# Kernel tuning notes

Hardware: AMD Instinct MI355X
Metric: run time of the kernel (lower is better)

## Reference

```python
import jax, jax.numpy as jnp
import numpy as np

T, H, E, K, I = 512, 2048, 16, 4, 1408
NS = 2
IS = I * NS  # shared-expert intermediate
SCALE = 1.0  # routed_scaling_factor


def setup_inputs() -> dict:
    key = jax.random.key(0)
    ks = jax.random.split(key, 6)
    init = lambda k, shape, fan: (jax.random.normal(k, shape, jnp.float32) * (fan ** -0.5))
    return {
        "hidden_states": jax.random.normal(ks[0], (T, H), jnp.float32),
        "gate_w": init(ks[1], (E, H), H),            # router weight
        "w_gate_up": init(ks[2], (E, 2 * I, H), H),  # merged gate_up per expert
        "w_down": init(ks[3], (E, H, I), I),         # down proj per expert
        "shared_gate_up": init(ks[4], (2 * IS, H), H),
        "shared_down": init(ks[5], (H, IS), IS),
    }


def reference(hidden_states, gate_w, w_gate_up, w_down, shared_gate_up, shared_down):
    x = hidden_states  # [T, H]
    # ---- shared experts (BailingMoEMLP: SiluAndMul) ----
    gu = x @ shared_gate_up.T                      # [T, 2*IS]
    g, u = jnp.split(gu, 2, axis=-1)
    shared = (jax.nn.silu(g) * u) @ shared_down.T  # [T, H]
    # ---- router: softmax scores, top-k, renormalize (norm_topk_prob=True) ----
    logits = x @ gate_w.T                          # [T, E]
    probs = jax.nn.softmax(logits, axis=-1)
    topk_w, topk_idx = jax.lax.top_k(probs, K)     # [T, K]
    topk_w = topk_w / jnp.sum(topk_w, axis=-1, keepdims=True)
    # dense combine weights [T, E] (scatter of top-k weights)
    t_idx = jnp.arange(x.shape[0])[:, None]
    cw = jnp.zeros((x.shape[0], E), x.dtype).at[t_idx, topk_idx].set(topk_w)
    # ---- experts: dense batched GEMM over all experts, weighted combine ----
    gu_e = jnp.einsum('th,eih->tei', x, w_gate_up)   # [T, E, 2I]
    g_e, u_e = jnp.split(gu_e, 2, axis=-1)
    h_e = jax.nn.silu(g_e) * u_e                     # [T, E, I]
    routed = jnp.einsum('tei,ehi,te->th', h_e, w_down, cw) * SCALE
    return routed + shared
```

## Files before the change

### kernel.cpp

```cpp
#include <hip/hip_runtime.h>
#include <hip/hip_bf16.h>
#include <math.h>

#define T_TOK 512
#define H_DIM 2048
#define E_NUM 16
#define K_TOP 4
#define I_DIM 1408
#define IS_DIM 2816

typedef __bf16 bf16;
typedef __attribute__((ext_vector_type(8))) __bf16 bf16x8;
typedef __attribute__((ext_vector_type(4))) float f32x4;

#define BM 64
#define BN 64
#define BK 64

__device__ inline bf16x8 cvt8(const float* __restrict__ p) {
    const f32x4 a = *(const f32x4*)(p);
    const f32x4 b = *(const f32x4*)(p + 4);
    bf16x8 r;
    r[0] = (bf16)a[0]; r[1] = (bf16)a[1]; r[2] = (bf16)a[2]; r[3] = (bf16)a[3];
    r[4] = (bf16)b[0]; r[5] = (bf16)b[1]; r[6] = (bf16)b[2]; r[7] = (bf16)b[3];
    return r;
}

__global__ __launch_bounds__(64) void router_kernel(
    const float* __restrict__ x, const float* __restrict__ gw,
    int* __restrict__ counts, int* __restrict__ tok_id, float* __restrict__ tok_w)
{
    int t = blockIdx.x;
    int lane = threadIdx.x;
    float acc[E_NUM];
#pragma unroll
    for (int e = 0; e < E_NUM; e++) acc[e] = 0.f;
    for (int h = lane; h < H_DIM; h += 64) {
        float xv = x[t * H_DIM + h];
#pragma unroll
        for (int e = 0; e < E_NUM; e++) acc[e] += xv * gw[e * H_DIM + h];
    }
#pragma unroll
    for (int e = 0; e < E_NUM; e++) {
#pragma unroll
        for (int off = 32; off; off >>= 1) acc[e] += __shfl_xor(acc[e], off);
    }
    if (lane == 0) {
        float m = acc[0];
#pragma unroll
        for (int e = 1; e < E_NUM; e++) m = fmaxf(m, acc[e]);
        float p[E_NUM];
#pragma unroll
        for (int e = 0; e < E_NUM; e++) p[e] = __expf(acc[e] - m);
        int sel[K_TOP];
        float pw[K_TOP];
        float wsum = 0.f;
        bool used[E_NUM];
#pragma unroll
        for (int e = 0; e < E_NUM; e++) used[e] = false;
        for (int k = 0; k < K_TOP; k++) {
            int best = 0;
            float bv = -1.f;
            for (int e = 0; e < E_NUM; e++) {
                if (!used[e] && p[e] > bv) { bv = p[e]; best = e; }
            }
            used[best] = true;
            sel[k] = best;
            pw[k] = bv;
            wsum += bv;
        }
        float inv = 1.f / wsum;
        for (int k = 0; k < K_TOP; k++) {
            int e = sel[k];
            int pos = atomicAdd(&counts[e], 1);
            tok_id[e * T_TOK + pos] = t;
            tok_w[e * T_TOK + pos] = pw[k] * inv;
        }
    }
}

template <bool GATHER>
__global__ __launch_bounds__(256) void gateup_kernel(
    const float* __restrict__ X,
    const float* __restrict__ W,
    long w_expert_stride,
    int pair_off_rows,
    bf16* __restrict__ Hout,
    long h_expert_stride,
    int ldh,
    const int* __restrict__ counts,
    const int* __restrict__ tok_id,
    const float* __restrict__ tok_w)
{
    int e = blockIdx.z;
    int n0 = blockIdx.x * BN;
    int m0 = blockIdx.y * BM;
    int count;
    if constexpr (GATHER) count = counts[e]; else count = T_TOK;
    if (m0 >= count) return;

    const float* Wg = W + (long)e * w_expert_stride;
    const float* Wu = Wg + (long)pair_off_rows * H_DIM;
    bf16* Ho = Hout + (long)e * h_expert_stride;
    const int* tid_p = nullptr;
    const float* tw_p = nullptr;
    if constexpr (GATHER) {
        tid_p = tok_id + e * T_TOK;
        tw_p = tok_w + e * T_TOK;
    }

    __shared__ bf16 sA[BM * BK];
    __shared__ bf16 sG[BN * BK];
    __shared__ bf16 sU[BN * BK];

    int tidx = threadIdx.x;
    int lane = tidx & 63;
    int wv = tidx >> 6;
    int wm = wv >> 1, wn = wv & 1;

    f32x4 accG[2][2], accU[2][2];
#pragma unroll
    for (int i = 0; i < 2; i++)
#pragma unroll
        for (int j = 0; j < 2; j++) {
            accG[i][j] = (f32x4){0.f, 0.f, 0.f, 0.f};
            accU[i][j] = (f32x4){0.f, 0.f, 0.f, 0.f};
        }

    long arow_off[2], wrow_off[2];
    int lds_off[2];
#pragma unroll
    for (int c2 = 0; c2 < 2; c2++) {
        int c = tidx + c2 * 256;
        int row = c >> 3, col8 = c & 7;
        int tok;
        if constexpr (GATHER) {
            int idx = m0 + row;
            tok = (idx < count) ? tid_p[idx] : tid_p[0];
        } else {
            tok = m0 + row;
        }
        arow_off[c2] = (long)tok * H_DIM + col8 * 8;
        wrow_off[c2] = (long)(n0 + row) * H_DIM + col8 * 8;
        lds_off[c2] = row * BK + ((col8 ^ (row & 7)) << 3);
    }

    const int ktiles = H_DIM / BK;
    for (int kt = 0; kt < ktiles; kt++) {
        int k0 = kt * BK;
#pragma unroll
        for (int c2 = 0; c2 < 2; c2++) {
            *(bf16x8*)&sA[lds_off[c2]] = cvt8(&X[arow_off[c2] + k0]);
            *(bf16x8*)&sG[lds_off[c2]] = cvt8(&Wg[wrow_off[c2] + k0]);
            *(bf16x8*)&sU[lds_off[c2]] = cvt8(&Wu[wrow_off[c2] + k0]);
        }
        __syncthreads();
        int quad = lane >> 4, l16 = lane & 15;
        bf16x8 aF[2][2], gF[2][2], uF[2][2];
#pragma unroll
        for (int mt = 0; mt < 2; mt++) {
            int r = wm * 32 + mt * 16 + l16;
            int rb = r * BK, rx = r & 7;
#pragma unroll
            for (int ks = 0; ks < 2; ks++)
                aF[mt][ks] = *(const bf16x8*)&sA[rb + (((ks * 4 + quad) ^ rx) << 3)];
        }
#pragma unroll
        for (int nt = 0; nt < 2; nt++) {
            int r = wn * 32 + nt * 16 + l16;
            int rb = r * BK, rx = r & 7;
#pragma unroll
            for (int ks = 0; ks < 2; ks++) {
                gF[nt][ks] = *(const bf16x8*)&sG[rb + (((ks * 4 + quad) ^ rx) << 3)];
                uF[nt][ks] = *(const bf16x8*)&sU[rb + (((ks * 4 + quad) ^ rx) << 3)];
            }
        }
#pragma unroll
        for (int ks = 0; ks < 2; ks++)
#pragma unroll
            for (int mt = 0; mt < 2; mt++)
#pragma unroll
                for (int nt = 0; nt < 2; nt++) {
                    accG[mt][nt] = __builtin_amdgcn_mfma_f32_16x16x32_bf16(aF[mt][ks], gF[nt][ks], accG[mt][nt], 0, 0, 0);
                    accU[mt][nt] = __builtin_amdgcn_mfma_f32_16x16x32_bf16(aF[mt][ks], uF[nt][ks], accU[mt][nt], 0, 0, 0);
                }
        __syncthreads();
    }

    int quad = lane >> 4, l16 = lane & 15;
#pragma unroll
    for (int mt = 0; mt < 2; mt++) {
#pragma unroll
        for (int r = 0; r < 4; r++) {
            int row = m0 + wm * 32 + mt * 16 + quad * 4 + r;
            if (row < count) {
                float wgt = 1.f;
                if constexpr (GATHER) wgt = tw_p[row];
#pragma unroll
                for (int nt = 0; nt < 2; nt++) {
                    int col = n0 + wn * 32 + nt * 16 + l16;
                    float g = accG[mt][nt][r];
                    float u = accU[mt][nt][r];
                    float sig = 1.f / (1.f + __expf(-g));
                    float h = g * sig * u * wgt;
                    Ho[(long)row * ldh + col] = (bf16)h;
                }
            }
        }
    }
}

template <bool GATHER>
__global__ __launch_bounds__(256) void down_kernel(
    const bf16* __restrict__ Hin,
    long h_expert_stride, int ldh, int Kdim,
    const float* __restrict__ W,
    long w_expert_stride,
    float* __restrict__ out,
    const int* __restrict__ counts,
    const int* __restrict__ tok_id)
{
    int e = blockIdx.z;
    int n0 = blockIdx.x * BN;
    int m0 = blockIdx.y * BM;
    int count;
    if constexpr (GATHER) count = counts[e]; else count = T_TOK;
    if (m0 >= count) return;

    const bf16* A = Hin + (long)e * h_expert_stride;
    const float* B = W + (long)e * w_expert_stride;
    const int* tid_p = nullptr;
    if constexpr (GATHER) tid_p = tok_id + e * T_TOK;

    __shared__ bf16 sA[BM * BK];
    __shared__ bf16 sB[BN * BK];

    int tidx = threadIdx.x;
    int lane = tidx & 63;
    int wv = tidx >> 6;
    int wm = wv >> 1, wn = wv & 1;

    f32x4 acc[2][2];
#pragma unroll
    for (int i = 0; i < 2; i++)
#pragma unroll
        for (int j = 0; j < 2; j++) acc[i][j] = (f32x4){0.f, 0.f, 0.f, 0.f};

    long arow_off[2], brow_off[2];
    int lds_off[2];
#pragma unroll
    for (int c2 = 0; c2 < 2; c2++) {
        int c = tidx + c2 * 256;
        int row = c >> 3, col8 = c & 7;
        arow_off[c2] = (long)(m0 + row) * ldh + col8 * 8;
        brow_off[c2] = (long)(n0 + row) * Kdim + col8 * 8;
        lds_off[c2] = row * BK + ((col8 ^ (row & 7)) << 3);
    }

    const int ktiles = Kdim / BK;
    for (int kt = 0; kt < ktiles; kt++) {
        int k0 = kt * BK;
#pragma unroll
        for (int c2 = 0; c2 < 2; c2++) {
            *(bf16x8*)&sA[lds_off[c2]] = *(const bf16x8*)&A[arow_off[c2] + k0];
            *(bf16x8*)&sB[lds_off[c2]] = cvt8(&B[brow_off[c2] + k0]);
        }
        __syncthreads();
        int quad = lane >> 4, l16 = lane & 15;
        bf16x8 aF[2][2], bF[2][2];
#pragma unroll
        for (int mt = 0; mt < 2; mt++) {
            int r = wm * 32 + mt * 16 + l16;
            int rb = r * BK, rx = r & 7;
#pragma unroll
            for (int ks = 0; ks < 2; ks++)
                aF[mt][ks] = *(const bf16x8*)&sA[rb + (((ks * 4 + quad) ^ rx) << 3)];
        }
#pragma unroll
        for (int nt = 0; nt < 2; nt++) {
            int r = wn * 32 + nt * 16 + l16;
            int rb = r * BK, rx = r & 7;
#pragma unroll
            for (int ks = 0; ks < 2; ks++)
                bF[nt][ks] = *(const bf16x8*)&sB[rb + (((ks * 4 + quad) ^ rx) << 3)];
        }
#pragma unroll
        for (int ks = 0; ks < 2; ks++)
#pragma unroll
            for (int mt = 0; mt < 2; mt++)
#pragma unroll
                for (int nt = 0; nt < 2; nt++)
                    acc[mt][nt] = __builtin_amdgcn_mfma_f32_16x16x32_bf16(aF[mt][ks], bF[nt][ks], acc[mt][nt], 0, 0, 0);
        __syncthreads();
    }

    int quad = lane >> 4, l16 = lane & 15;
#pragma unroll
    for (int mt = 0; mt < 2; mt++) {
#pragma unroll
        for (int r = 0; r < 4; r++) {
            int row = m0 + wm * 32 + mt * 16 + quad * 4 + r;
            if (row < count) {
#pragma unroll
                for (int nt = 0; nt < 2; nt++) {
                    int col = n0 + wn * 32 + nt * 16 + l16;
                    float v = acc[mt][nt][r];
                    if constexpr (GATHER) {
                        int tok = tid_p[row];
                        atomicAdd(&out[(long)tok * H_DIM + col], v);
                    } else {
                        out[(long)row * H_DIM + col] = v;
                    }
                }
            }
        }
    }
}

extern "C" void kernel_launch(void* const* d_in, const int* in_sizes, int n_in,
                              void* d_out, int out_size, void* d_ws, size_t ws_size,
                              hipStream_t stream)
{
    const float* x              = (const float*)d_in[0];
    const float* gate_w         = (const float*)d_in[1];
    const float* w_gate_up      = (const float*)d_in[2];
    const float* w_down         = (const float*)d_in[3];
    const float* shared_gate_up = (const float*)d_in[4];
    const float* shared_down    = (const float*)d_in[5];
    float* out = (float*)d_out;

    char* ws = (char*)d_ws;
    int*   counts  = (int*)(ws + 0);
    int*   tok_id  = (int*)(ws + 256);
    float* tok_w   = (float*)(ws + 33024);
    bf16*  hshared = (bf16*)(ws + 65792);
    bf16*  hrouted = (bf16*)(ws + 2949376);

    hipMemsetAsync(counts, 0, E_NUM * sizeof(int), stream);

    router_kernel<<<T_TOK, 64, 0, stream>>>(x, gate_w, counts, tok_id, tok_w);

    gateup_kernel<false><<<dim3(IS_DIM / BN, T_TOK / BM, 1), 256, 0, stream>>>(
        x, shared_gate_up, 0L, IS_DIM, hshared, 0L, IS_DIM, nullptr, nullptr, nullptr);

    gateup_kernel<true><<<dim3(I_DIM / BN, T_TOK / BM, E_NUM), 256, 0, stream>>>(
        x, w_gate_up, (long)2 * I_DIM * H_DIM, I_DIM, hrouted, (long)T_TOK * I_DIM, I_DIM,
        counts, tok_id, tok_w);

    down_kernel<false><<<dim3(H_DIM / BN, T_TOK / BM, 1), 256, 0, stream>>>(
        hshared, 0L, IS_DIM, IS_DIM, shared_down, 0L, out, nullptr, nullptr);

    down_kernel<true><<<dim3(H_DIM / BN, T_TOK / BM, E_NUM), 256, 0, stream>>>(
        hrouted, (long)T_TOK * I_DIM, I_DIM, I_DIM, w_down, (long)H_DIM * I_DIM, out,
        counts, tok_id);
}
```

Baseline: 859.1 us.

## Prefetch next K-tile into registers in gate-up and down GEMM kernels

Both GEMM kernels now load the next K tile from global memory into registers while the current tile's MFMAs run. Before, each iteration loaded and converted its tile just before the barrier. The end-of-loop barrier moves to the start of the loop, so the LDS store of the prefetched data still waits for the previous compute. Launch bounds also gain minimum occupancy hints (2 for gate-up, 3 for down), which could force register spills given the extra prefetch registers.

```diff
diff --git a/kernel.cpp b/kernel.cpp
--- a/kernel.cpp
+++ b/kernel.cpp
@@ -17,9 +17,7 @@
 #define BN 64
 #define BK 64
 
-__device__ inline bf16x8 cvt8(const float* __restrict__ p) {
-    const f32x4 a = *(const f32x4*)(p);
-    const f32x4 b = *(const f32x4*)(p + 4);
+__device__ inline bf16x8 cvt8v(f32x4 a, f32x4 b) {
     bf16x8 r;
     r[0] = (bf16)a[0]; r[1] = (bf16)a[1]; r[2] = (bf16)a[2]; r[3] = (bf16)a[3];
     r[4] = (bf16)b[0]; r[5] = (bf16)b[1]; r[6] = (bf16)b[2]; r[7] = (bf16)b[3];
@@ -80,7 +78,7 @@
 }
 
 template <bool GATHER>
-__global__ __launch_bounds__(256) void gateup_kernel(
+__global__ __launch_bounds__(256, 2) void gateup_kernel(
     const float* __restrict__ X,
     const float* __restrict__ W,
     long w_expert_stride,
@@ -145,14 +143,37 @@
         lds_off[c2] = row * BK + ((col8 ^ (row & 7)) << 3);
     }
 
+    f32x4 pA[2][2], pG[2][2], pU[2][2];
+#pragma unroll
+    for (int c2 = 0; c2 < 2; c2++) {
+        pA[c2][0] = *(const f32x4*)&X[arow_off[c2]];
+        pA[c2][1] = *(const f32x4*)&X[arow_off[c2] + 4];
+        pG[c2][0] = *(const f32x4*)&Wg[wrow_off[c2]];
+        pG[c2][1] = *(const f32x4*)&Wg[wrow_off[c2] + 4];
+        pU[c2][0] = *(const f32x4*)&Wu[wrow_off[c2]];
+        pU[c2][1] = *(const f32x4*)&Wu[wrow_off[c2] + 4];
+    }
+
     const int ktiles = H_DIM / BK;
     for (int kt = 0; kt < ktiles; kt++) {
-        int k0 = kt * BK;
+        __syncthreads();
 #pragma unroll
         for (int c2 = 0; c2 < 2; c2++) {
-            *(bf16x8*)&sA[lds_off[c2]] = cvt8(&X[arow_off[c2] + k0]);
-            *(bf16x8*)&sG[lds_off[c2]] = cvt8(&Wg[wrow_off[c2] + k0]);
-            *(bf16x8*)&sU[lds_off[c2]] = cvt8(&Wu[wrow_off[c2] + k0]);
+            *(bf16x8*)&sA[lds_off[c2]] = cvt8v(pA[c2][0], pA[c2][1]);
+            *(bf16x8*)&sG[lds_off[c2]] = cvt8v(pG[c2][0], pG[c2][1]);
+            *(bf16x8*)&sU[lds_off[c2]] = cvt8v(pU[c2][0], pU[c2][1]);
+        }
+        {
+            int k0n = (kt + 1 < ktiles) ? (kt + 1) * BK : kt * BK;
+#pragma unroll
+            for (int c2 = 0; c2 < 2; c2++) {
+                pA[c2][0] = *(const f32x4*)&X[arow_off[c2] + k0n];
+                pA[c2][1] = *(const f32x4*)&X[arow_off[c2] + k0n + 4];
+                pG[c2][0] = *(const f32x4*)&Wg[wrow_off[c2] + k0n];
+                pG[c2][1] = *(const f32x4*)&Wg[wrow_off[c2] + k0n + 4];
+                pU[c2][0] = *(const f32x4*)&Wu[wrow_off[c2] + k0n];
+                pU[c2][1] = *(const f32x4*)&Wu[wrow_off[c2] + k0n + 4];
+            }
         }
         __syncthreads();
         int quad = lane >> 4, l16 = lane & 15;
@@ -184,7 +205,6 @@
                     accG[mt][nt] = __builtin_amdgcn_mfma_f32_16x16x32_bf16(aF[mt][ks], gF[nt][ks], accG[mt][nt], 0, 0, 0);
                     accU[mt][nt] = __builtin_amdgcn_mfma_f32_16x16x32_bf16(aF[mt][ks], uF[nt][ks], accU[mt][nt], 0, 0, 0);
                 }
-        __syncthreads();
     }
 
     int quad = lane >> 4, l16 = lane & 15;
@@ -211,7 +231,7 @@
 }
 
 template <bool GATHER>
-__global__ __launch_bounds__(256) void down_kernel(
+__global__ __launch_bounds__(256, 3) void down_kernel(
     const bf16* __restrict__ Hin,
     long h_expert_stride, int ldh, int Kdim,
     const float* __restrict__ W,
@@ -257,13 +277,31 @@
         lds_off[c2] = row * BK + ((col8 ^ (row & 7)) << 3);
     }
 
+    bf16x8 pA[2];
+    f32x4 pB[2][2];
+#pragma unroll
+    for (int c2 = 0; c2 < 2; c2++) {
+        pA[c2] = *(const bf16x8*)&A[arow_off[c2]];
+        pB[c2][0] = *(const f32x4*)&B[brow_off[c2]];
+        pB[c2][1] = *(const f32x4*)&B[brow_off[c2] + 4];
+    }
+
     const int ktiles = Kdim / BK;
     for (int kt = 0; kt < ktiles; kt++) {
-        int k0 = kt * BK;
+        __syncthreads();
 #pragma unroll
         for (int c2 = 0; c2 < 2; c2++) {
-            *(bf16x8*)&sA[lds_off[c2]] = *(const bf16x8*)&A[arow_off[c2] + k0];
-            *(bf16x8*)&sB[lds_off[c2]] = cvt8(&B[brow_off[c2] + k0]);
+            *(bf16x8*)&sA[lds_off[c2]] = pA[c2];
+            *(bf16x8*)&sB[lds_off[c2]] = cvt8v(pB[c2][0], pB[c2][1]);
+        }
+        {
+            int k0n = (kt + 1 < ktiles) ? (kt + 1) * BK : kt * BK;
+#pragma unroll
+            for (int c2 = 0; c2 < 2; c2++) {
+                pA[c2] = *(const bf16x8*)&A[arow_off[c2] + k0n];
+                pB[c2][0] = *(const f32x4*)&B[brow_off[c2] + k0n];
+                pB[c2][1] = *(const f32x4*)&B[brow_off[c2] + k0n + 4];
+            }
         }
         __syncthreads();
         int quad = lane >> 4, l16 = lane & 15;
@@ -291,7 +329,6 @@
 #pragma unroll
                 for (int nt = 0; nt < 2; nt++)
                     acc[mt][nt] = __builtin_amdgcn_mfma_f32_16x16x32_bf16(aF[mt][ks], bF[nt][ks], acc[mt][nt], 0, 0, 0);
-        __syncthreads();
     }
 
     int quad = lane >> 4, l16 = lane & 15;
```

Result: no change. 847.0 us (-1.4%).
